# Optimization experiments

Hardware: AMD Instinct MI355X
Metric: run time of the kernel (lower is better)

## Reference

```python
import jax, jax.numpy as jnp
import numpy as np

B, N, D = 4096, 64, 256  # batch, n_nodes, d_input


def setup_inputs() -> dict:
    key = jax.random.key(0)
    k = jax.random.split(key, 6)
    return {
        "x": jax.random.normal(k[0], (B, N, D), dtype=jnp.float32),
        "W1": jax.random.normal(k[1], (1,), dtype=jnp.float32),
        "W2": jax.random.normal(k[2], (D, 1), dtype=jnp.float32),
        "W3": jax.random.normal(k[3], (D,), dtype=jnp.float32),
        "bs": jax.random.normal(k[4], (1, N, N), dtype=jnp.float32),
        "Vs": jax.random.normal(k[5], (N, N), dtype=jnp.float32),
    }


def reference(x, W1, W2, W3, bs, Vs):
    # x: (B, N, D). Dropout is identity (inference / p=0).
    # LHS = (x * W1) @ W2  -> (B, N, 1); collapse to (B, N)
    lhs = jnp.einsum("bnd,d->bn", x, W2[:, 0]) * W1[0]
    # RHS = W3 @ x (over feature dim) -> (B, N); used as (B, 1, N)
    rhs = jnp.einsum("bnd,d->bn", x, W3)
    # scores: Vs @ tanh(outer(lhs, rhs) + bs)  -> (B, N, N)
    t = jnp.tanh(lhs[:, :, None] * rhs[:, None, :] + bs)  # (B, N, N)
    s = jnp.einsum("ij,bjk->bik", Vs, t)  # (B, N, N)
    # softmax over the flattened N*N scores per batch element
    a = jax.nn.softmax(s.reshape(x.shape[0], -1), axis=-1)
    return a.reshape(-1, N, N)
```

## Files before the change

kernel.cpp:

```cpp
#include <hip/hip_runtime.h>


typedef float f32x4 __attribute__((ext_vector_type(4)));
typedef __bf16 bf16x8 __attribute__((ext_vector_type(8)));

__global__ __launch_bounds__(256, 6) void adjatt_kernel(
    const float* __restrict__ x,
    const float* __restrict__ W1,
    const float* __restrict__ W2,
    const float* __restrict__ W3,
    const float* __restrict__ bs,
    const float* __restrict__ Vs,
    float* __restrict__ out)
{
    __shared__ __align__(16) unsigned char tT[16384];
    __shared__ __align__(16) float lhs[64];
    __shared__ __align__(16) float rhs[64];
    __shared__ float redm[4], reds[4];

    const int tid  = threadIdx.x;
    const int b    = blockIdx.x;
    const int lane = tid & 63;
    const int w    = tid >> 6;
    const float W1v = W1[0];

    {
        const int r = tid >> 2;
        const int q = tid & 3;
        const float* xr  = x + (size_t)b * 16384 + r * 256 + q * 4;
        const float* w2p = W2 + q * 4;
        const float* w3p = W3 + q * 4;
        float d2 = 0.f, d3 = 0.f;
        #pragma unroll 4
        for (int c = 0; c < 16; ++c) {
            f32x4 xv = *(const f32x4*)(xr + c * 16);
            f32x4 w2 = *(const f32x4*)(w2p + c * 16);
            f32x4 w3 = *(const f32x4*)(w3p + c * 16);
            d2 = fmaf(xv[0], w2[0], d2); d2 = fmaf(xv[1], w2[1], d2);
            d2 = fmaf(xv[2], w2[2], d2); d2 = fmaf(xv[3], w2[3], d2);
            d3 = fmaf(xv[0], w3[0], d3); d3 = fmaf(xv[1], w3[1], d3);
            d3 = fmaf(xv[2], w3[2], d3); d3 = fmaf(xv[3], w3[3], d3);
        }
        d2 += __shfl_xor(d2, 1); d2 += __shfl_xor(d2, 2);
        d3 += __shfl_xor(d3, 1); d3 += __shfl_xor(d3, 2);
        if (q == 0) { lhs[r] = d2 * W1v; rhs[r] = d3; }
    }
    __syncthreads();

    bf16x8 Vh[2], Vl[2];
    {
        const int row = 16 * w + (lane & 15);
        #pragma unroll
        for (int s = 0; s < 2; ++s) {
            const float* vp = Vs + row * 64 + 32 * s + 8 * (lane >> 4);
            f32x4 f0 = *(const f32x4*)vp;
            f32x4 f1 = *(const f32x4*)(vp + 4);
            #pragma unroll
            for (int e = 0; e < 4; ++e) {
                __bf16 h0 = (__bf16)f0[e];
                Vh[s][e] = h0;
                Vl[s][e] = (__bf16)(f0[e] - (float)h0);
                __bf16 h1 = (__bf16)f1[e];
                Vh[s][e + 4] = h1;
                Vl[s][e + 4] = (__bf16)(f1[e] - (float)h1);
            }
        }
    }

    {
        const int n  = lane;
        const int j0 = 16 * w;
        const float rv = rhs[n];
        f32x4 lh[4];
        #pragma unroll
        for (int c = 0; c < 4; ++c) lh[c] = *(const f32x4*)&lhs[j0 + 4 * c];
        bf16x8 hi[2], lo[2];
        #pragma unroll
        for (int jj = 0; jj < 16; ++jj) {
            float z  = fmaf(lh[jj >> 2][jj & 3], rv, bs[(j0 + jj) * 64 + n]);
            float e2 = __expf(2.f * z);
            float th = 1.f - __fdividef(2.f, e2 + 1.f);
            __bf16 h = (__bf16)th;
            hi[jj >> 3][jj & 7] = h;
            lo[jj >> 3][jj & 7] = (__bf16)(th - (float)h);
        }
        #pragma unroll
        for (int c = 0; c < 2; ++c) {
            const int off = (n * 128 + (j0 + 8 * c) * 2) ^ ((n & 7) << 4);
            *(bf16x8*)(tT + off)        = hi[c];
            *(bf16x8*)(tT + 8192 + off) = lo[c];
        }
    }
    __syncthreads();

    f32x4 acc[4];
    #pragma unroll
    for (int ct = 0; ct < 4; ++ct) acc[ct] = (f32x4){0.f, 0.f, 0.f, 0.f};
    #pragma unroll
    for (int ct = 0; ct < 4; ++ct) {
        const int n = 16 * ct + (lane & 15);
        #pragma unroll
        for (int sk = 0; sk < 2; ++sk) {
            const int off = (n * 128 + 64 * sk + 16 * (lane >> 4)) ^ ((n & 7) << 4);
            bf16x8 Th = *(const bf16x8*)(tT + off);
            bf16x8 Tl = *(const bf16x8*)(tT + 8192 + off);
            acc[ct] = __builtin_amdgcn_mfma_f32_16x16x32_bf16(Th, Vh[sk], acc[ct], 0, 0, 0);
            acc[ct] = __builtin_amdgcn_mfma_f32_16x16x32_bf16(Tl, Vh[sk], acc[ct], 0, 0, 0);
            acc[ct] = __builtin_amdgcn_mfma_f32_16x16x32_bf16(Th, Vl[sk], acc[ct], 0, 0, 0);
        }
    }

    float m = acc[0][0];
    #pragma unroll
    for (int ct = 0; ct < 4; ++ct)
        #pragma unroll
        for (int e = 0; e < 4; ++e) m = fmaxf(m, acc[ct][e]);
    #pragma unroll
    for (int off = 1; off < 64; off <<= 1) m = fmaxf(m, __shfl_xor(m, off));
    if (lane == 0) redm[w] = m;
    __syncthreads();
    const float M = fmaxf(fmaxf(redm[0], redm[1]), fmaxf(redm[2], redm[3]));

    float ssum = 0.f;
    #pragma unroll
    for (int ct = 0; ct < 4; ++ct)
        #pragma unroll
        for (int e = 0; e < 4; ++e) {
            acc[ct][e] = __expf(acc[ct][e] - M);
            ssum += acc[ct][e];
        }
    #pragma unroll
    for (int off = 1; off < 64; off <<= 1) ssum += __shfl_xor(ssum, off);
    if (lane == 0) reds[w] = ssum;
    __syncthreads();
    const float inv = __fdividef(1.f, reds[0] + reds[1] + reds[2] + reds[3]);

    float* ob = out + (size_t)b * 4096 + (16 * w + (lane & 15)) * 64 + 4 * (lane >> 4);
    #pragma unroll
    for (int ct = 0; ct < 4; ++ct) {
        f32x4 v = {acc[ct][0] * inv, acc[ct][1] * inv, acc[ct][2] * inv, acc[ct][3] * inv};
        *(f32x4*)(ob + 16 * ct) = v;
    }
}

extern "C" void kernel_launch(void* const* d_in, const int* in_sizes, int n_in,
                              void* d_out, int out_size, void* d_ws, size_t ws_size,
                              hipStream_t stream) {
    const float* x  = (const float*)d_in[0];
    const float* W1 = (const float*)d_in[1];
    const float* W2 = (const float*)d_in[2];
    const float* W3 = (const float*)d_in[3];
    const float* bs = (const float*)d_in[4];
    const float* Vs = (const float*)d_in[5];
    float* out = (float*)d_out;

    const int B = in_sizes[0] / (64 * 256);
    adjatt_kernel<<<dim3(B), dim3(256), 0, stream>>>(x, W1, W2, W3, bs, Vs, out);
}
```

Measured before the change: 74.54 us.

## Halve block to 128 threads, each wave computing two row tiles

Shrinks the block from four waves to two, so each wave now produces 32 output rows (two 16-row MFMA tiles) and does two rows of the x dot-product pass. Each loaded T fragment from LDS is reused across two V row tiles, which halves LDS fragment reads per MFMA. The Vs conversion is also moved ahead of the x pass so it can overlap with those loads. In exchange there are fewer waves per batch element, more registers per thread and longer serial work per wave, which may reduce the latency hiding during the memory-bound x load.

```diff
diff --git a/kernel.cpp b/kernel.cpp
--- a/kernel.cpp
+++ b/kernel.cpp
@@ -4,7 +4,7 @@
 typedef float f32x4 __attribute__((ext_vector_type(4)));
 typedef __bf16 bf16x8 __attribute__((ext_vector_type(8)));
 
-__global__ __launch_bounds__(256, 6) void adjatt_kernel(
+__global__ __launch_bounds__(128, 4) void adjatt_kernel(
     const float* __restrict__ x,
     const float* __restrict__ W1,
     const float* __restrict__ W2,
@@ -16,7 +16,7 @@
     __shared__ __align__(16) unsigned char tT[16384];
     __shared__ __align__(16) float lhs[64];
     __shared__ __align__(16) float rhs[64];
-    __shared__ float redm[4], reds[4];
+    __shared__ float redm[2], reds[2];
 
     const int tid  = threadIdx.x;
     const int b    = blockIdx.x;
@@ -24,78 +24,86 @@
     const int w    = tid >> 6;
     const float W1v = W1[0];
 
-    {
-        const int r = tid >> 2;
-        const int q = tid & 3;
-        const float* xr  = x + (size_t)b * 16384 + r * 256 + q * 4;
-        const float* w2p = W2 + q * 4;
-        const float* w3p = W3 + q * 4;
-        float d2 = 0.f, d3 = 0.f;
-        #pragma unroll 4
-        for (int c = 0; c < 16; ++c) {
-            f32x4 xv = *(const f32x4*)(xr + c * 16);
-            f32x4 w2 = *(const f32x4*)(w2p + c * 16);
-            f32x4 w3 = *(const f32x4*)(w3p + c * 16);
-            d2 = fmaf(xv[0], w2[0], d2); d2 = fmaf(xv[1], w2[1], d2);
-            d2 = fmaf(xv[2], w2[2], d2); d2 = fmaf(xv[3], w2[3], d2);
-            d3 = fmaf(xv[0], w3[0], d3); d3 = fmaf(xv[1], w3[1], d3);
-            d3 = fmaf(xv[2], w3[2], d3); d3 = fmaf(xv[3], w3[3], d3);
-        }
-        d2 += __shfl_xor(d2, 1); d2 += __shfl_xor(d2, 2);
-        d3 += __shfl_xor(d3, 1); d3 += __shfl_xor(d3, 2);
-        if (q == 0) { lhs[r] = d2 * W1v; rhs[r] = d3; }
-    }
-    __syncthreads();
-
-    bf16x8 Vh[2], Vl[2];
-    {
-        const int row = 16 * w + (lane & 15);
+    bf16x8 Vh[2][2], Vl[2][2];
+    #pragma unroll
+    for (int rt = 0; rt < 2; ++rt) {
+        const int row = 32 * w + 16 * rt + (lane & 15);
         #pragma unroll
-        for (int s = 0; s < 2; ++s) {
-            const float* vp = Vs + row * 64 + 32 * s + 8 * (lane >> 4);
+        for (int sk = 0; sk < 2; ++sk) {
+            const float* vp = Vs + row * 64 + 32 * sk + 8 * (lane >> 4);
             f32x4 f0 = *(const f32x4*)vp;
             f32x4 f1 = *(const f32x4*)(vp + 4);
             #pragma unroll
             for (int e = 0; e < 4; ++e) {
                 __bf16 h0 = (__bf16)f0[e];
-                Vh[s][e] = h0;
-                Vl[s][e] = (__bf16)(f0[e] - (float)h0);
+                Vh[rt][sk][e] = h0;
+                Vl[rt][sk][e] = (__bf16)(f0[e] - (float)h0);
                 __bf16 h1 = (__bf16)f1[e];
-                Vh[s][e + 4] = h1;
-                Vl[s][e + 4] = (__bf16)(f1[e] - (float)h1);
+                Vh[rt][sk][e + 4] = h1;
+                Vl[rt][sk][e + 4] = (__bf16)(f1[e] - (float)h1);
             }
         }
     }
 
     {
-        const int n  = lane;
-        const int j0 = 16 * w;
-        const float rv = rhs[n];
-        f32x4 lh[4];
+        const int q  = tid & 3;
+        const int r0 = tid >> 2;
         #pragma unroll
-        for (int c = 0; c < 4; ++c) lh[c] = *(const f32x4*)&lhs[j0 + 4 * c];
-        bf16x8 hi[2], lo[2];
-        #pragma unroll
-        for (int jj = 0; jj < 16; ++jj) {
-            float z  = fmaf(lh[jj >> 2][jj & 3], rv, bs[(j0 + jj) * 64 + n]);
-            float e2 = __expf(2.f * z);
-            float th = 1.f - __fdividef(2.f, e2 + 1.f);
-            __bf16 h = (__bf16)th;
-            hi[jj >> 3][jj & 7] = h;
-            lo[jj >> 3][jj & 7] = (__bf16)(th - (float)h);
-        }
-        #pragma unroll
-        for (int c = 0; c < 2; ++c) {
-            const int off = (n * 128 + (j0 + 8 * c) * 2) ^ ((n & 7) << 4);
-            *(bf16x8*)(tT + off)        = hi[c];
-            *(bf16x8*)(tT + 8192 + off) = lo[c];
+        for (int pass = 0; pass < 2; ++pass) {
+            const int r = 32 * pass + r0;
+            const float* xr  = x + (size_t)b * 16384 + r * 256 + q * 4;
+            const float* w2p = W2 + q * 4;
+            const float* w3p = W3 + q * 4;
+            float d2 = 0.f, d3 = 0.f;
+            #pragma unroll 4
+            for (int c = 0; c < 16; ++c) {
+                f32x4 xv = *(const f32x4*)(xr + c * 16);
+                f32x4 w2 = *(const f32x4*)(w2p + c * 16);
+                f32x4 w3 = *(const f32x4*)(w3p + c * 16);
+                d2 = fmaf(xv[0], w2[0], d2); d2 = fmaf(xv[1], w2[1], d2);
+                d2 = fmaf(xv[2], w2[2], d2); d2 = fmaf(xv[3], w2[3], d2);
+                d3 = fmaf(xv[0], w3[0], d3); d3 = fmaf(xv[1], w3[1], d3);
+                d3 = fmaf(xv[2], w3[2], d3); d3 = fmaf(xv[3], w3[3], d3);
+            }
+            d2 += __shfl_xor(d2, 1); d2 += __shfl_xor(d2, 2);
+            d3 += __shfl_xor(d3, 1); d3 += __shfl_xor(d3, 2);
+            if (q == 0) { lhs[r] = d2 * W1v; rhs[r] = d3; }
         }
     }
     __syncthreads();
 
-    f32x4 acc[4];
+    {
+        const int n  = lane;
+        const int j0 = 32 * w;
+        const float rv = rhs[n];
+        #pragma unroll
+        for (int c = 0; c < 4; ++c) {
+            const int jb = j0 + 8 * c;
+            f32x4 l0 = *(const f32x4*)&lhs[jb];
+            f32x4 l1 = *(const f32x4*)&lhs[jb + 4];
+            bf16x8 hi, lo;
+            #pragma unroll
+            for (int jj = 0; jj < 8; ++jj) {
+                const float lj = (jj < 4) ? l0[jj & 3] : l1[jj & 3];
+                float z  = fmaf(lj, rv, bs[(jb + jj) * 64 + n]);
+                float e2 = __expf(2.f * z);
+                float th = 1.f - __fdividef(2.f, e2 + 1.f);
+                __bf16 h = (__bf16)th;
+                hi[jj] = h;
+                lo[jj] = (__bf16)(th - (float)h);
+            }
+            const int off = (n * 128 + jb * 2) ^ ((n & 7) << 4);
+            *(bf16x8*)(tT + off)        = hi;
+            *(bf16x8*)(tT + 8192 + off) = lo;
+        }
+    }
+    __syncthreads();
+
+    f32x4 acc[2][4];
     #pragma unroll
-    for (int ct = 0; ct < 4; ++ct) acc[ct] = (f32x4){0.f, 0.f, 0.f, 0.f};
+    for (int rt = 0; rt < 2; ++rt)
+        #pragma unroll
+        for (int ct = 0; ct < 4; ++ct) acc[rt][ct] = (f32x4){0.f, 0.f, 0.f, 0.f};
     #pragma unroll
     for (int ct = 0; ct < 4; ++ct) {
         const int n = 16 * ct + (lane & 15);
@@ -104,42 +112,54 @@
             const int off = (n * 128 + 64 * sk + 16 * (lane >> 4)) ^ ((n & 7) << 4);
             bf16x8 Th = *(const bf16x8*)(tT + off);
             bf16x8 Tl = *(const bf16x8*)(tT + 8192 + off);
-            acc[ct] = __builtin_amdgcn_mfma_f32_16x16x32_bf16(Th, Vh[sk], acc[ct], 0, 0, 0);
-            acc[ct] = __builtin_amdgcn_mfma_f32_16x16x32_bf16(Tl, Vh[sk], acc[ct], 0, 0, 0);
-            acc[ct] = __builtin_amdgcn_mfma_f32_16x16x32_bf16(Th, Vl[sk], acc[ct], 0, 0, 0);
+            #pragma unroll
+            for (int rt = 0; rt < 2; ++rt) {
+                acc[rt][ct] = __builtin_amdgcn_mfma_f32_16x16x32_bf16(Th, Vh[rt][sk], acc[rt][ct], 0, 0, 0);
+                acc[rt][ct] = __builtin_amdgcn_mfma_f32_16x16x32_bf16(Tl, Vh[rt][sk], acc[rt][ct], 0, 0, 0);
+                acc[rt][ct] = __builtin_amdgcn_mfma_f32_16x16x32_bf16(Th, Vl[rt][sk], acc[rt][ct], 0, 0, 0);
+            }
         }
     }
 
-    float m = acc[0][0];
+    float m = acc[0][0][0];
     #pragma unroll
-    for (int ct = 0; ct < 4; ++ct)
+    for (int rt = 0; rt < 2; ++rt)
         #pragma unroll
-        for (int e = 0; e < 4; ++e) m = fmaxf(m, acc[ct][e]);
+        for (int ct = 0; ct < 4; ++ct)
+            #pragma unroll
+            for (int e = 0; e < 4; ++e) m = fmaxf(m, acc[rt][ct][e]);
     #pragma unroll
     for (int off = 1; off < 64; off <<= 1) m = fmaxf(m, __shfl_xor(m, off));
     if (lane == 0) redm[w] = m;
     __syncthreads();
-    const float M = fmaxf(fmaxf(redm[0], redm[1]), fmaxf(redm[2], redm[3]));
+    const float M = fmaxf(redm[0], redm[1]);
 
     float ssum = 0.f;
     #pragma unroll
-    for (int ct = 0; ct < 4; ++ct)
+    for (int rt = 0; rt < 2; ++rt)
         #pragma unroll
-        for (int e = 0; e < 4; ++e) {
-            acc[ct][e] = __expf(acc[ct][e] - M);
-            ssum += acc[ct][e];
-        }
+        for (int ct = 0; ct < 4; ++ct)
+            #pragma unroll
+            for (int e = 0; e < 4; ++e) {
+                acc[rt][ct][e] = __expf(acc[rt][ct][e] - M);
+                ssum += acc[rt][ct][e];
+            }
     #pragma unroll
     for (int off = 1; off < 64; off <<= 1) ssum += __shfl_xor(ssum, off);
     if (lane == 0) reds[w] = ssum;
     __syncthreads();
-    const float inv = __fdividef(1.f, reds[0] + reds[1] + reds[2] + reds[3]);
+    const float inv = __fdividef(1.f, reds[0] + reds[1]);
 
-    float* ob = out + (size_t)b * 4096 + (16 * w + (lane & 15)) * 64 + 4 * (lane >> 4);
     #pragma unroll
-    for (int ct = 0; ct < 4; ++ct) {
-        f32x4 v = {acc[ct][0] * inv, acc[ct][1] * inv, acc[ct][2] * inv, acc[ct][3] * inv};
-        *(f32x4*)(ob + 16 * ct) = v;
+    for (int rt = 0; rt < 2; ++rt) {
+        float* ob = out + (size_t)b * 4096 +
+                    (32 * w + 16 * rt + (lane & 15)) * 64 + 4 * (lane >> 4);
+        #pragma unroll
+        for (int ct = 0; ct < 4; ++ct) {
+            f32x4 v = {acc[rt][ct][0] * inv, acc[rt][ct][1] * inv,
+                       acc[rt][ct][2] * inv, acc[rt][ct][3] * inv};
+            *(f32x4*)(ob + 16 * ct) = v;
+        }
     }
 }
 
@@ -155,5 +175,5 @@
     float* out = (float*)d_out;
 
     const int B = in_sizes[0] / (64 * 256);
-    adjatt_kernel<<<dim3(B), dim3(256), 0, stream>>>(x, W1, W2, W3, bs, Vs, out);
+    adjatt_kernel<<<dim3(B), dim3(128), 0, stream>>>(x, W1, W2, W3, bs, Vs, out);
 }
```

Result: slower. 79.70 us (+6.9%).

## Process four batch elements per block with register-prefetched x

Applied to the files above, without the earlier changes.

Each block now loops over four batch elements. W2/W3 and the bf16 split of Vs are set up once per block, and W2/W3 are staged in shared memory. The next element's x slice is prefetched into 16 f32x4 registers while the current element's MFMA and softmax run, so global load latency overlaps compute. The price is higher register pressure (launch bounds lowered to 4 waves per SIMD), a grid four times smaller, and a possible tail imbalance across CUs.

```diff
diff --git a/kernel.cpp b/kernel.cpp
--- a/kernel.cpp
+++ b/kernel.cpp
@@ -4,142 +4,182 @@
 typedef float f32x4 __attribute__((ext_vector_type(4)));
 typedef __bf16 bf16x8 __attribute__((ext_vector_type(8)));
 
-__global__ __launch_bounds__(256, 6) void adjatt_kernel(
+constexpr int NB = 4;
+
+__global__ __launch_bounds__(256, 4) void adjatt_kernel(
     const float* __restrict__ x,
     const float* __restrict__ W1,
     const float* __restrict__ W2,
     const float* __restrict__ W3,
     const float* __restrict__ bs,
     const float* __restrict__ Vs,
-    float* __restrict__ out)
+    float* __restrict__ out,
+    int B)
 {
     __shared__ __align__(16) unsigned char tT[16384];
     __shared__ __align__(16) float lhs[64];
     __shared__ __align__(16) float rhs[64];
+    __shared__ __align__(16) float w2l[256];
+    __shared__ __align__(16) float w3l[256];
     __shared__ float redm[4], reds[4];
 
     const int tid  = threadIdx.x;
-    const int b    = blockIdx.x;
     const int lane = tid & 63;
     const int w    = tid >> 6;
     const float W1v = W1[0];
 
-    {
-        const int r = tid >> 2;
-        const int q = tid & 3;
-        const float* xr  = x + (size_t)b * 16384 + r * 256 + q * 4;
-        const float* w2p = W2 + q * 4;
-        const float* w3p = W3 + q * 4;
-        float d2 = 0.f, d3 = 0.f;
-        #pragma unroll 4
-        for (int c = 0; c < 16; ++c) {
-            f32x4 xv = *(const f32x4*)(xr + c * 16);
-            f32x4 w2 = *(const f32x4*)(w2p + c * 16);
-            f32x4 w3 = *(const f32x4*)(w3p + c * 16);
-            d2 = fmaf(xv[0], w2[0], d2); d2 = fmaf(xv[1], w2[1], d2);
-            d2 = fmaf(xv[2], w2[2], d2); d2 = fmaf(xv[3], w2[3], d2);
-            d3 = fmaf(xv[0], w3[0], d3); d3 = fmaf(xv[1], w3[1], d3);
-            d3 = fmaf(xv[2], w3[2], d3); d3 = fmaf(xv[3], w3[3], d3);
-        }
-        d2 += __shfl_xor(d2, 1); d2 += __shfl_xor(d2, 2);
-        d3 += __shfl_xor(d3, 1); d3 += __shfl_xor(d3, 2);
-        if (q == 0) { lhs[r] = d2 * W1v; rhs[r] = d3; }
-    }
-    __syncthreads();
+    const int b0 = blockIdx.x * NB;
+    const int nb = (B - b0 < NB) ? (B - b0) : NB;
+
+    w2l[tid] = W2[tid];
+    w3l[tid] = W3[tid];
 
     bf16x8 Vh[2], Vl[2];
     {
         const int row = 16 * w + (lane & 15);
         #pragma unroll
-        for (int s = 0; s < 2; ++s) {
-            const float* vp = Vs + row * 64 + 32 * s + 8 * (lane >> 4);
+        for (int sk = 0; sk < 2; ++sk) {
+            const float* vp = Vs + row * 64 + 32 * sk + 8 * (lane >> 4);
             f32x4 f0 = *(const f32x4*)vp;
             f32x4 f1 = *(const f32x4*)(vp + 4);
             #pragma unroll
             for (int e = 0; e < 4; ++e) {
                 __bf16 h0 = (__bf16)f0[e];
-                Vh[s][e] = h0;
-                Vl[s][e] = (__bf16)(f0[e] - (float)h0);
+                Vh[sk][e] = h0;
+                Vl[sk][e] = (__bf16)(f0[e] - (float)h0);
                 __bf16 h1 = (__bf16)f1[e];
-                Vh[s][e + 4] = h1;
-                Vl[s][e + 4] = (__bf16)(f1[e] - (float)h1);
+                Vh[sk][e + 4] = h1;
+                Vl[sk][e + 4] = (__bf16)(f1[e] - (float)h1);
             }
         }
     }
 
-    {
-        const int n  = lane;
-        const int j0 = 16 * w;
-        const float rv = rhs[n];
-        f32x4 lh[4];
-        #pragma unroll
-        for (int c = 0; c < 4; ++c) lh[c] = *(const f32x4*)&lhs[j0 + 4 * c];
-        bf16x8 hi[2], lo[2];
-        #pragma unroll
-        for (int jj = 0; jj < 16; ++jj) {
-            float z  = fmaf(lh[jj >> 2][jj & 3], rv, bs[(j0 + jj) * 64 + n]);
-            float e2 = __expf(2.f * z);
-            float th = 1.f - __fdividef(2.f, e2 + 1.f);
-            __bf16 h = (__bf16)th;
-            hi[jj >> 3][jj & 7] = h;
-            lo[jj >> 3][jj & 7] = (__bf16)(th - (float)h);
-        }
-        #pragma unroll
-        for (int c = 0; c < 2; ++c) {
-            const int off = (n * 128 + (j0 + 8 * c) * 2) ^ ((n & 7) << 4);
-            *(bf16x8*)(tT + off)        = hi[c];
-            *(bf16x8*)(tT + 8192 + off) = lo[c];
-        }
-    }
+    const int co = tid & 15;
+    const int r0 = tid >> 4;
+    const float* xbase = x + (size_t)b0 * 16384 + r0 * 256 + co * 4;
+
+    f32x4 xp[16];
+    #pragma unroll
+    for (int it = 0; it < 4; ++it)
+        #pragma unroll
+        for (int kk = 0; kk < 4; ++kk)
+            xp[it * 4 + kk] = *(const f32x4*)(xbase + it * 4096 + kk * 64);
+
     __syncthreads();
 
-    f32x4 acc[4];
-    #pragma unroll
-    for (int ct = 0; ct < 4; ++ct) acc[ct] = (f32x4){0.f, 0.f, 0.f, 0.f};
-    #pragma unroll
-    for (int ct = 0; ct < 4; ++ct) {
-        const int n = 16 * ct + (lane & 15);
-        #pragma unroll
-        for (int sk = 0; sk < 2; ++sk) {
-            const int off = (n * 128 + 64 * sk + 16 * (lane >> 4)) ^ ((n & 7) << 4);
-            bf16x8 Th = *(const bf16x8*)(tT + off);
-            bf16x8 Tl = *(const bf16x8*)(tT + 8192 + off);
-            acc[ct] = __builtin_amdgcn_mfma_f32_16x16x32_bf16(Th, Vh[sk], acc[ct], 0, 0, 0);
-            acc[ct] = __builtin_amdgcn_mfma_f32_16x16x32_bf16(Tl, Vh[sk], acc[ct], 0, 0, 0);
-            acc[ct] = __builtin_amdgcn_mfma_f32_16x16x32_bf16(Th, Vl[sk], acc[ct], 0, 0, 0);
-        }
-    }
-
-    float m = acc[0][0];
-    #pragma unroll
-    for (int ct = 0; ct < 4; ++ct)
-        #pragma unroll
-        for (int e = 0; e < 4; ++e) m = fmaxf(m, acc[ct][e]);
-    #pragma unroll
-    for (int off = 1; off < 64; off <<= 1) m = fmaxf(m, __shfl_xor(m, off));
-    if (lane == 0) redm[w] = m;
-    __syncthreads();
-    const float M = fmaxf(fmaxf(redm[0], redm[1]), fmaxf(redm[2], redm[3]));
-
-    float ssum = 0.f;
-    #pragma unroll
-    for (int ct = 0; ct < 4; ++ct)
-        #pragma unroll
-        for (int e = 0; e < 4; ++e) {
-            acc[ct][e] = __expf(acc[ct][e] - M);
-            ssum += acc[ct][e];
-        }
-    #pragma unroll
-    for (int off = 1; off < 64; off <<= 1) ssum += __shfl_xor(ssum, off);
-    if (lane == 0) reds[w] = ssum;
-    __syncthreads();
-    const float inv = __fdividef(1.f, reds[0] + reds[1] + reds[2] + reds[3]);
-
-    float* ob = out + (size_t)b * 4096 + (16 * w + (lane & 15)) * 64 + 4 * (lane >> 4);
-    #pragma unroll
-    for (int ct = 0; ct < 4; ++ct) {
-        f32x4 v = {acc[ct][0] * inv, acc[ct][1] * inv, acc[ct][2] * inv, acc[ct][3] * inv};
-        *(f32x4*)(ob + 16 * ct) = v;
+    for (int k = 0; k < nb; ++k) {
+        const int b = b0 + k;
+
+        {
+            f32x4 wv2[4], wv3[4];
+            #pragma unroll
+            for (int kk = 0; kk < 4; ++kk) {
+                wv2[kk] = *(const f32x4*)&w2l[4 * (co + 16 * kk)];
+                wv3[kk] = *(const f32x4*)&w3l[4 * (co + 16 * kk)];
+            }
+            #pragma unroll
+            for (int it = 0; it < 4; ++it) {
+                float d2 = 0.f, d3 = 0.f;
+                #pragma unroll
+                for (int kk = 0; kk < 4; ++kk) {
+                    f32x4 xv = xp[it * 4 + kk];
+                    d2 = fmaf(xv[0], wv2[kk][0], d2); d2 = fmaf(xv[1], wv2[kk][1], d2);
+                    d2 = fmaf(xv[2], wv2[kk][2], d2); d2 = fmaf(xv[3], wv2[kk][3], d2);
+                    d3 = fmaf(xv[0], wv3[kk][0], d3); d3 = fmaf(xv[1], wv3[kk][1], d3);
+                    d3 = fmaf(xv[2], wv3[kk][2], d3); d3 = fmaf(xv[3], wv3[kk][3], d3);
+                }
+                d2 += __shfl_xor(d2, 1); d2 += __shfl_xor(d2, 2);
+                d2 += __shfl_xor(d2, 4); d2 += __shfl_xor(d2, 8);
+                d3 += __shfl_xor(d3, 1); d3 += __shfl_xor(d3, 2);
+                d3 += __shfl_xor(d3, 4); d3 += __shfl_xor(d3, 8);
+                if (co == 0) { lhs[r0 + 16 * it] = d2 * W1v; rhs[r0 + 16 * it] = d3; }
+            }
+        }
+        __syncthreads();
+
+        {
+            const int n  = lane;
+            const int j0 = 16 * w;
+            const float rv = rhs[n];
+            f32x4 lh[4];
+            #pragma unroll
+            for (int c = 0; c < 4; ++c) lh[c] = *(const f32x4*)&lhs[j0 + 4 * c];
+            bf16x8 hi[2], lo[2];
+            #pragma unroll
+            for (int jj = 0; jj < 16; ++jj) {
+                float z  = fmaf(lh[jj >> 2][jj & 3], rv, bs[(j0 + jj) * 64 + n]);
+                float e2 = __expf(2.f * z);
+                float th = 1.f - __fdividef(2.f, e2 + 1.f);
+                __bf16 h = (__bf16)th;
+                hi[jj >> 3][jj & 7] = h;
+                lo[jj >> 3][jj & 7] = (__bf16)(th - (float)h);
+            }
+            #pragma unroll
+            for (int c = 0; c < 2; ++c) {
+                const int off = (n * 128 + (j0 + 8 * c) * 2) ^ ((n & 7) << 4);
+                *(bf16x8*)(tT + off)        = hi[c];
+                *(bf16x8*)(tT + 8192 + off) = lo[c];
+            }
+        }
+        __syncthreads();
+
+        if (k + 1 < nb) {
+            const float* xn = xbase + (size_t)(k + 1) * 16384;
+            #pragma unroll
+            for (int it = 0; it < 4; ++it)
+                #pragma unroll
+                for (int kk = 0; kk < 4; ++kk)
+                    xp[it * 4 + kk] = *(const f32x4*)(xn + it * 4096 + kk * 64);
+        }
+
+        f32x4 acc[4];
+        #pragma unroll
+        for (int ct = 0; ct < 4; ++ct) acc[ct] = (f32x4){0.f, 0.f, 0.f, 0.f};
+        #pragma unroll
+        for (int ct = 0; ct < 4; ++ct) {
+            const int n = 16 * ct + (lane & 15);
+            #pragma unroll
+            for (int sk = 0; sk < 2; ++sk) {
+                const int off = (n * 128 + 64 * sk + 16 * (lane >> 4)) ^ ((n & 7) << 4);
+                bf16x8 Th = *(const bf16x8*)(tT + off);
+                bf16x8 Tl = *(const bf16x8*)(tT + 8192 + off);
+                acc[ct] = __builtin_amdgcn_mfma_f32_16x16x32_bf16(Th, Vh[sk], acc[ct], 0, 0, 0);
+                acc[ct] = __builtin_amdgcn_mfma_f32_16x16x32_bf16(Tl, Vh[sk], acc[ct], 0, 0, 0);
+                acc[ct] = __builtin_amdgcn_mfma_f32_16x16x32_bf16(Th, Vl[sk], acc[ct], 0, 0, 0);
+            }
+        }
+
+        float m = acc[0][0];
+        #pragma unroll
+        for (int ct = 0; ct < 4; ++ct)
+            #pragma unroll
+            for (int e = 0; e < 4; ++e) m = fmaxf(m, acc[ct][e]);
+        #pragma unroll
+        for (int off = 1; off < 64; off <<= 1) m = fmaxf(m, __shfl_xor(m, off));
+        if (lane == 0) redm[w] = m;
+        __syncthreads();
+        const float M = fmaxf(fmaxf(redm[0], redm[1]), fmaxf(redm[2], redm[3]));
+
+        float ssum = 0.f;
+        #pragma unroll
+        for (int ct = 0; ct < 4; ++ct)
+            #pragma unroll
+            for (int e = 0; e < 4; ++e) {
+                acc[ct][e] = __expf(acc[ct][e] - M);
+                ssum += acc[ct][e];
+            }
+        #pragma unroll
+        for (int off = 1; off < 64; off <<= 1) ssum += __shfl_xor(ssum, off);
+        if (lane == 0) reds[w] = ssum;
+        __syncthreads();
+        const float inv = __fdividef(1.f, reds[0] + reds[1] + reds[2] + reds[3]);
+
+        float* ob = out + (size_t)b * 4096 + (16 * w + (lane & 15)) * 64 + 4 * (lane >> 4);
+        #pragma unroll
+        for (int ct = 0; ct < 4; ++ct) {
+            f32x4 v = {acc[ct][0] * inv, acc[ct][1] * inv, acc[ct][2] * inv, acc[ct][3] * inv};
+            *(f32x4*)(ob + 16 * ct) = v;
+        }
     }
 }
 
@@ -155,5 +195,6 @@
     float* out = (float*)d_out;
 
     const int B = in_sizes[0] / (64 * 256);
-    adjatt_kernel<<<dim3(B), dim3(256), 0, stream>>>(x, W1, W2, W3, bs, Vs, out);
+    const int grid = (B + NB - 1) / NB;
+    adjatt_kernel<<<dim3(grid), dim3(256), 0, stream>>>(x, W1, W2, W3, bs, Vs, out, B);
 }
```

Measured after the change: 121.9 us. 63.6% more time.

## Process one batch element per wavefront, removing shared memory and block barriers

Applied to the files above, without the earlier changes.

Each wavefront now handles a whole batch element, not four wavefronts sharing one. The tanh tile is computed directly in MFMA operand registers instead of being staged through LDS, and lhs/rhs are exchanged via shuffles. This removes LDS traffic and __syncthreads. In exchange each wave holds 64 accumulator floats plus the V fragments, raising register pressure, so launch bounds drop to 3 blocks, and the bs and Vs loads plus the V split are repeated per wave.

```diff
diff --git a/kernel.cpp b/kernel.cpp
--- a/kernel.cpp
+++ b/kernel.cpp
@@ -4,143 +4,146 @@
 typedef float f32x4 __attribute__((ext_vector_type(4)));
 typedef __bf16 bf16x8 __attribute__((ext_vector_type(8)));
 
-__global__ __launch_bounds__(256, 6) void adjatt_kernel(
+__global__ __launch_bounds__(256, 3) void adjatt_kernel(
     const float* __restrict__ x,
     const float* __restrict__ W1,
     const float* __restrict__ W2,
     const float* __restrict__ W3,
     const float* __restrict__ bs,
     const float* __restrict__ Vs,
-    float* __restrict__ out)
+    float* __restrict__ out,
+    int B)
 {
-    __shared__ __align__(16) unsigned char tT[16384];
-    __shared__ __align__(16) float lhs[64];
-    __shared__ __align__(16) float rhs[64];
-    __shared__ float redm[4], reds[4];
+    const int tid = threadIdx.x;
+    const int l   = tid & 63;
+    const int wv  = tid >> 6;
+    const int b   = blockIdx.x * 4 + wv;
+    if (b >= B) return;
 
-    const int tid  = threadIdx.x;
-    const int b    = blockIdx.x;
-    const int lane = tid & 63;
-    const int w    = tid >> 6;
     const float W1v = W1[0];
+    const int l15 = l & 15;
+    const int eb  = 8 * (l >> 4);
 
+    float lhsv = 0.f, rhsv = 0.f;
     {
-        const int r = tid >> 2;
-        const int q = tid & 3;
-        const float* xr  = x + (size_t)b * 16384 + r * 256 + q * 4;
-        const float* w2p = W2 + q * 4;
-        const float* w3p = W3 + q * 4;
-        float d2 = 0.f, d3 = 0.f;
-        #pragma unroll 4
-        for (int c = 0; c < 16; ++c) {
-            f32x4 xv = *(const f32x4*)(xr + c * 16);
-            f32x4 w2 = *(const f32x4*)(w2p + c * 16);
-            f32x4 w3 = *(const f32x4*)(w3p + c * 16);
-            d2 = fmaf(xv[0], w2[0], d2); d2 = fmaf(xv[1], w2[1], d2);
-            d2 = fmaf(xv[2], w2[2], d2); d2 = fmaf(xv[3], w2[3], d2);
-            d3 = fmaf(xv[0], w3[0], d3); d3 = fmaf(xv[1], w3[1], d3);
-            d3 = fmaf(xv[2], w3[2], d3); d3 = fmaf(xv[3], w3[3], d3);
+        const int rs = l & 3;
+        const int cg = l >> 2;
+        f32x4 w2v[4], w3v[4];
+        #pragma unroll
+        for (int cc = 0; cc < 4; ++cc) {
+            w2v[cc] = *(const f32x4*)(W2 + cg * 4 + 64 * cc);
+            w3v[cc] = *(const f32x4*)(W3 + cg * 4 + 64 * cc);
         }
-        d2 += __shfl_xor(d2, 1); d2 += __shfl_xor(d2, 2);
-        d3 += __shfl_xor(d3, 1); d3 += __shfl_xor(d3, 2);
-        if (q == 0) { lhs[r] = d2 * W1v; rhs[r] = d3; }
+        const float* xb = x + (size_t)b * 16384 + rs * 256 + cg * 4;
+        #pragma unroll
+        for (int it = 0; it < 16; ++it) {
+            const float* xr = xb + it * 1024;
+            float d2 = 0.f, d3 = 0.f;
+            #pragma unroll
+            for (int cc = 0; cc < 4; ++cc) {
+                f32x4 xv = *(const f32x4*)(xr + 64 * cc);
+                d2 = fmaf(xv[0], w2v[cc][0], d2); d2 = fmaf(xv[1], w2v[cc][1], d2);
+                d2 = fmaf(xv[2], w2v[cc][2], d2); d2 = fmaf(xv[3], w2v[cc][3], d2);
+                d3 = fmaf(xv[0], w3v[cc][0], d3); d3 = fmaf(xv[1], w3v[cc][1], d3);
+                d3 = fmaf(xv[2], w3v[cc][2], d3); d3 = fmaf(xv[3], w3v[cc][3], d3);
+            }
+            d2 += __shfl_xor(d2, 4);  d2 += __shfl_xor(d2, 8);
+            d2 += __shfl_xor(d2, 16); d2 += __shfl_xor(d2, 32);
+            d3 += __shfl_xor(d3, 4);  d3 += __shfl_xor(d3, 8);
+            d3 += __shfl_xor(d3, 16); d3 += __shfl_xor(d3, 32);
+            if (cg == it) { lhsv = d2 * W1v; rhsv = d3; }
+        }
     }
-    __syncthreads();
 
-    bf16x8 Vh[2], Vl[2];
-    {
-        const int row = 16 * w + (lane & 15);
+    float rn[4];
+    #pragma unroll
+    for (int ct = 0; ct < 4; ++ct) rn[ct] = __shfl(rhsv, 16 * ct + l15);
+
+    f32x4 acc[4][4];
+    #pragma unroll
+    for (int rb = 0; rb < 4; ++rb)
         #pragma unroll
-        for (int s = 0; s < 2; ++s) {
-            const float* vp = Vs + row * 64 + 32 * s + 8 * (lane >> 4);
+        for (int ct = 0; ct < 4; ++ct) acc[rb][ct] = (f32x4){0.f, 0.f, 0.f, 0.f};
+
+    #pragma unroll
+    for (int sk = 0; sk < 2; ++sk) {
+        float lj[8];
+        #pragma unroll
+        for (int e = 0; e < 8; ++e) lj[e] = __shfl(lhsv, 32 * sk + eb + e);
+
+        bf16x8 Th[4], Tl[4];
+        #pragma unroll
+        for (int ct = 0; ct < 4; ++ct) {
+            const int n = 16 * ct + l15;
+            const float* bsp = bs + (32 * sk + eb) * 64 + n;
+            #pragma unroll
+            for (int e = 0; e < 8; ++e) {
+                float z  = fmaf(lj[e], rn[ct], bsp[e * 64]);
+                float e2 = __expf(2.f * z);
+                float th = 1.f - __fdividef(2.f, e2 + 1.f);
+                __bf16 h = (__bf16)th;
+                Th[ct][e] = h;
+                Tl[ct][e] = (__bf16)(th - (float)h);
+            }
+        }
+
+        #pragma unroll
+        for (int rb = 0; rb < 4; ++rb) {
+            const float* vp = Vs + (16 * rb + l15) * 64 + 32 * sk + eb;
             f32x4 f0 = *(const f32x4*)vp;
             f32x4 f1 = *(const f32x4*)(vp + 4);
+            bf16x8 Vh, Vl;
             #pragma unroll
             for (int e = 0; e < 4; ++e) {
                 __bf16 h0 = (__bf16)f0[e];
-                Vh[s][e] = h0;
-                Vl[s][e] = (__bf16)(f0[e] - (float)h0);
+                Vh[e] = h0;
+                Vl[e] = (__bf16)(f0[e] - (float)h0);
                 __bf16 h1 = (__bf16)f1[e];
-                Vh[s][e + 4] = h1;
-                Vl[s][e + 4] = (__bf16)(f1[e] - (float)h1);
+                Vh[e + 4] = h1;
+                Vl[e + 4] = (__bf16)(f1[e] - (float)h1);
+            }
+            #pragma unroll
+            for (int ct = 0; ct < 4; ++ct) {
+                acc[rb][ct] = __builtin_amdgcn_mfma_f32_16x16x32_bf16(Th[ct], Vh, acc[rb][ct], 0, 0, 0);
+                acc[rb][ct] = __builtin_amdgcn_mfma_f32_16x16x32_bf16(Tl[ct], Vh, acc[rb][ct], 0, 0, 0);
+                acc[rb][ct] = __builtin_amdgcn_mfma_f32_16x16x32_bf16(Th[ct], Vl, acc[rb][ct], 0, 0, 0);
             }
         }
     }
 
-    {
-        const int n  = lane;
-        const int j0 = 16 * w;
-        const float rv = rhs[n];
-        f32x4 lh[4];
+    float m = acc[0][0][0];
+    #pragma unroll
+    for (int rb = 0; rb < 4; ++rb)
         #pragma unroll
-        for (int c = 0; c < 4; ++c) lh[c] = *(const f32x4*)&lhs[j0 + 4 * c];
-        bf16x8 hi[2], lo[2];
-        #pragma unroll
-        for (int jj = 0; jj < 16; ++jj) {
-            float z  = fmaf(lh[jj >> 2][jj & 3], rv, bs[(j0 + jj) * 64 + n]);
-            float e2 = __expf(2.f * z);
-            float th = 1.f - __fdividef(2.f, e2 + 1.f);
-            __bf16 h = (__bf16)th;
-            hi[jj >> 3][jj & 7] = h;
-            lo[jj >> 3][jj & 7] = (__bf16)(th - (float)h);
-        }
-        #pragma unroll
-        for (int c = 0; c < 2; ++c) {
-            const int off = (n * 128 + (j0 + 8 * c) * 2) ^ ((n & 7) << 4);
-            *(bf16x8*)(tT + off)        = hi[c];
-            *(bf16x8*)(tT + 8192 + off) = lo[c];
-        }
-    }
-    __syncthreads();
-
-    f32x4 acc[4];
-    #pragma unroll
-    for (int ct = 0; ct < 4; ++ct) acc[ct] = (f32x4){0.f, 0.f, 0.f, 0.f};
-    #pragma unroll
-    for (int ct = 0; ct < 4; ++ct) {
-        const int n = 16 * ct + (lane & 15);
-        #pragma unroll
-        for (int sk = 0; sk < 2; ++sk) {
-            const int off = (n * 128 + 64 * sk + 16 * (lane >> 4)) ^ ((n & 7) << 4);
-            bf16x8 Th = *(const bf16x8*)(tT + off);
-            bf16x8 Tl = *(const bf16x8*)(tT + 8192 + off);
-            acc[ct] = __builtin_amdgcn_mfma_f32_16x16x32_bf16(Th, Vh[sk], acc[ct], 0, 0, 0);
-            acc[ct] = __builtin_amdgcn_mfma_f32_16x16x32_bf16(Tl, Vh[sk], acc[ct], 0, 0, 0);
-            acc[ct] = __builtin_amdgcn_mfma_f32_16x16x32_bf16(Th, Vl[sk], acc[ct], 0, 0, 0);
-        }
-    }
-
-    float m = acc[0][0];
-    #pragma unroll
-    for (int ct = 0; ct < 4; ++ct)
-        #pragma unroll
-        for (int e = 0; e < 4; ++e) m = fmaxf(m, acc[ct][e]);
+        for (int ct = 0; ct < 4; ++ct)
+            #pragma unroll
+            for (int e = 0; e < 4; ++e) m = fmaxf(m, acc[rb][ct][e]);
     #pragma unroll
     for (int off = 1; off < 64; off <<= 1) m = fmaxf(m, __shfl_xor(m, off));
-    if (lane == 0) redm[w] = m;
-    __syncthreads();
-    const float M = fmaxf(fmaxf(redm[0], redm[1]), fmaxf(redm[2], redm[3]));
 
     float ssum = 0.f;
     #pragma unroll
-    for (int ct = 0; ct < 4; ++ct)
+    for (int rb = 0; rb < 4; ++rb)
         #pragma unroll
-        for (int e = 0; e < 4; ++e) {
-            acc[ct][e] = __expf(acc[ct][e] - M);
-            ssum += acc[ct][e];
-        }
+        for (int ct = 0; ct < 4; ++ct)
+            #pragma unroll
+            for (int e = 0; e < 4; ++e) {
+                acc[rb][ct][e] = __expf(acc[rb][ct][e] - m);
+                ssum += acc[rb][ct][e];
+            }
     #pragma unroll
     for (int off = 1; off < 64; off <<= 1) ssum += __shfl_xor(ssum, off);
-    if (lane == 0) reds[w] = ssum;
-    __syncthreads();
-    const float inv = __fdividef(1.f, reds[0] + reds[1] + reds[2] + reds[3]);
+    const float inv = __fdividef(1.f, ssum);
 
-    float* ob = out + (size_t)b * 4096 + (16 * w + (lane & 15)) * 64 + 4 * (lane >> 4);
+    float* ob = out + (size_t)b * 4096 + l15 * 64 + 4 * (l >> 4);
     #pragma unroll
-    for (int ct = 0; ct < 4; ++ct) {
-        f32x4 v = {acc[ct][0] * inv, acc[ct][1] * inv, acc[ct][2] * inv, acc[ct][3] * inv};
-        *(f32x4*)(ob + 16 * ct) = v;
-    }
+    for (int rb = 0; rb < 4; ++rb)
+        #pragma unroll
+        for (int ct = 0; ct < 4; ++ct) {
+            f32x4 v = {acc[rb][ct][0] * inv, acc[rb][ct][1] * inv,
+                       acc[rb][ct][2] * inv, acc[rb][ct][3] * inv};
+            *(f32x4*)(ob + rb * 1024 + ct * 16) = v;
+        }
 }
 
 extern "C" void kernel_launch(void* const* d_in, const int* in_sizes, int n_in,
@@ -155,5 +158,6 @@
     float* out = (float*)d_out;
 
     const int B = in_sizes[0] / (64 * 256);
-    adjatt_kernel<<<dim3(B), dim3(256), 0, stream>>>(x, W1, W2, W3, bs, Vs, out);
+    const int grid = (B + 3) / 4;
+    adjatt_kernel<<<dim3(grid), dim3(256), 0, stream>>>(x, W1, W2, W3, bs, Vs, out, B);
 }
```

Result: slower. 82.03 us (+10.1%).
